# Optimization experiments

Hardware: AMD Instinct MI355X
Metric: run time of the kernel (lower is better)

The kernel has to match this reference:

```python
import jax, jax.numpy as jnp
import numpy as np

N_NODES = 100000
N_EDGES = 1600000
D = 256
N_QUERY = 50000

def setup_inputs() -> dict:
    key = jax.random.key(0)
    k1, k2, k3, k4, k5, k6 = jax.random.split(key, 6)
    embeddings = jax.random.normal(k1, (N_NODES, D), dtype=jnp.float32)
    edge_src = jax.random.randint(k2, (N_EDGES,), 0, N_NODES)
    edge_dst = jax.random.randint(k3, (N_EDGES,), 0, N_NODES)
    edge_w = jax.random.uniform(k4, (N_EDGES,), dtype=jnp.float32)
    node_ids = jax.random.randint(k5, (N_QUERY,), 0, N_NODES)
    # Xavier-uniform linear weight, zero bias (as in _init_weights)
    limit = float(np.sqrt(6.0 / (D + D)))
    W = jax.random.uniform(k6, (D, D), dtype=jnp.float32, minval=-limit, maxval=limit)
    b = jnp.zeros((D,), dtype=jnp.float32)
    return {"embeddings": embeddings, "edge_src": edge_src, "edge_dst": edge_dst,
            "edge_w": edge_w, "node_ids": node_ids, "W": W, "b": b}

def reference(embeddings, edge_src, edge_dst, edge_w, node_ids, W, b):
    # graph_convolution: sparse adj (COO) @ embeddings == scatter-add of weighted src rows into dst
    msgs = embeddings[edge_src] * edge_w[:, None]                # [E, D]
    agg = jax.ops.segment_sum(msgs, edge_dst, num_segments=N_NODES)  # [N, D]
    # predict_scores: gather queried nodes, apply linear classifier
    feats = agg[node_ids]                                        # [Q, D]
    return feats @ W.T + b                                       # [Q, D]
```

## Files before the change

### kernel.cpp

```cpp
#include <hip/hip_runtime.h>

#define D 256
#define TQ 32
#define GQ 64
#define NBW 3136

typedef __attribute__((ext_vector_type(8))) short short8;
typedef __attribute__((ext_vector_type(4))) short short4v;
typedef __attribute__((ext_vector_type(4))) float f32x4;

__device__ __forceinline__ unsigned short f2bf(float x) {
    unsigned int u = __float_as_uint(x);
    unsigned int r = (u + 0x7FFFu + ((u >> 16) & 1u)) >> 16;
    return (unsigned short)r;
}
__device__ __forceinline__ float bf2f(unsigned short h) {
    return __uint_as_float(((unsigned int)h) << 16);
}


__global__ __launch_bounds__(256) void convert_emb(
    const float4* __restrict__ emb, short8* __restrict__ embbf, int total8)
{
    int stride = gridDim.x * 256;
    for (int i = blockIdx.x * 256 + threadIdx.x; i < total8; i += stride) {
        float4 v0 = emb[(size_t)i * 2 + 0];
        float4 v1 = emb[(size_t)i * 2 + 1];
        short8 p;
        p[0] = (short)f2bf(v0.x); p[1] = (short)f2bf(v0.y);
        p[2] = (short)f2bf(v0.z); p[3] = (short)f2bf(v0.w);
        p[4] = (short)f2bf(v1.x); p[5] = (short)f2bf(v1.y);
        p[6] = (short)f2bf(v1.z); p[7] = (short)f2bf(v1.w);
        embbf[i] = p;
    }
}

__global__ __launch_bounds__(256) void convert_w(
    const float* __restrict__ W, unsigned short* __restrict__ Wbf)
{
    int i = blockIdx.x * 256 + threadIdx.x;
    const float4* src = (const float4*)W + (size_t)i * 2;
    float4 v0 = src[0];
    float4 v1 = src[1];
    short8 p;
    p[0] = (short)f2bf(v0.x); p[1] = (short)f2bf(v0.y);
    p[2] = (short)f2bf(v0.z); p[3] = (short)f2bf(v0.w);
    p[4] = (short)f2bf(v1.x); p[5] = (short)f2bf(v1.y);
    p[6] = (short)f2bf(v1.z); p[7] = (short)f2bf(v1.w);
    *((short8*)Wbf + i) = p;
}


__global__ __launch_bounds__(256) void flag_bits(
    const int* __restrict__ nid, unsigned int* __restrict__ bits, int Q)
{
    int q = blockIdx.x * 256 + threadIdx.x;
    if (q < Q) {
        int v = nid[q];
        atomicOr(&bits[v >> 5], 1u << (v & 31));
    }
}

__global__ __launch_bounds__(256) void hist_kernel(
    const int* __restrict__ edst, const unsigned int* __restrict__ bits,
    int* __restrict__ counts, int E)
{
    __shared__ unsigned int lb[NBW];
    for (int i = threadIdx.x; i < NBW; i += 256) lb[i] = bits[i];
    __syncthreads();
    int stride = gridDim.x * 256;
    for (int e = blockIdx.x * 256 + threadIdx.x; e < E; e += stride) {
        int d = edst[e];
        if ((lb[d >> 5] >> (d & 31)) & 1u) atomicAdd(&counts[d], 1);
    }
}

__global__ __launch_bounds__(256) void alloc_kernel(
    const int* __restrict__ counts, int* __restrict__ base,
    int* __restrict__ pos, int* __restrict__ total, int N)
{
    int n = blockIdx.x * 256 + threadIdx.x;
    if (n >= N) return;
    int c = counts[n];
    int b = 0;
    if (c > 0) b = atomicAdd(total, c);
    base[n] = b;
    pos[n]  = b;
}

__global__ __launch_bounds__(256) void bucket_kernel(
    const int* __restrict__ esrc, const int* __restrict__ edst,
    const float* __restrict__ ew, const unsigned int* __restrict__ bits,
    int* __restrict__ pos, int2* __restrict__ bucket, int E)
{
    __shared__ unsigned int lb[NBW];
    for (int i = threadIdx.x; i < NBW; i += 256) lb[i] = bits[i];
    __syncthreads();
    int stride = gridDim.x * 256;
    for (int e = blockIdx.x * 256 + threadIdx.x; e < E; e += stride) {
        int d = edst[e];
        if ((lb[d >> 5] >> (d & 31)) & 1u) {
            int idx = atomicAdd(&pos[d], 1);
            bucket[idx] = make_int2(esrc[e], __float_as_int(ew[e]));
        }
    }
}

__global__ __launch_bounds__(256) void accum_nodes(
    const short4v* __restrict__ embbf,
    const int2*    __restrict__ bucket,
    const int*     __restrict__ base,
    const int*     __restrict__ counts,
    const unsigned int* __restrict__ bits,
    short4v*       __restrict__ aggbf,
    int N)
{
    const int lane = threadIdx.x & 63;
    const int wid  = (int)((blockIdx.x * 256 + threadIdx.x) >> 6);
    if (wid >= N) return;
    if (!((bits[wid >> 5] >> (wid & 31)) & 1u)) return;

    const int b = base[wid];
    const int c = counts[wid];
    float a0 = 0.f, a1 = 0.f, a2 = 0.f, a3 = 0.f;

    int i = 0;
    for (; i + 8 <= c; i += 8) {
        #pragma unroll
        for (int u = 0; u < 8; ++u) {
            int2 s = bucket[b + i + u];
            short4v v = embbf[(size_t)s.x * 64 + lane];
            float w = __int_as_float(s.y);
            a0 += bf2f((unsigned short)v[0]) * w;
            a1 += bf2f((unsigned short)v[1]) * w;
            a2 += bf2f((unsigned short)v[2]) * w;
            a3 += bf2f((unsigned short)v[3]) * w;
        }
    }
    for (; i < c; ++i) {
        int2 s = bucket[b + i];
        short4v v = embbf[(size_t)s.x * 64 + lane];
        float w = __int_as_float(s.y);
        a0 += bf2f((unsigned short)v[0]) * w;
        a1 += bf2f((unsigned short)v[1]) * w;
        a2 += bf2f((unsigned short)v[2]) * w;
        a3 += bf2f((unsigned short)v[3]) * w;
    }
    short4v o;
    o[0] = (short)f2bf(a0); o[1] = (short)f2bf(a1);
    o[2] = (short)f2bf(a2); o[3] = (short)f2bf(a3);
    aggbf[(size_t)wid * 64 + lane] = o;
}

__global__ __launch_bounds__(256) void gather_gemm_mfma(
    const unsigned short* __restrict__ aggbf,
    const int* __restrict__ nid,
    const unsigned short* __restrict__ Wbf,
    const float* __restrict__ b,
    float* __restrict__ out, int Q)
{
    __shared__ unsigned char lds[GQ * 512];
    const int t  = threadIdx.x;
    const int q0 = blockIdx.x * GQ;

    #pragma unroll
    for (int s = 0; s < 8; ++s) {
        const int i   = t + s * 256;
        const int row = i >> 5;
        const int ch  = i & 31;
        const int q   = q0 + row;
        short8 p = {0, 0, 0, 0, 0, 0, 0, 0};
        if (q < Q) p = *((const short8*)aggbf + (size_t)nid[q] * 32 + ch);
        int byte = row * 512 + ch * 16;
        byte ^= (row & 7) << 4;
        *(short8*)(lds + byte) = p;
    }
    __syncthreads();

    const int wave = t >> 6;
    const int lane = t & 63;
    const int qw   = wave * 16;
    const int lrow = lane & 15;
    const int kg   = lane >> 4;

    short8 afrag[8];
    #pragma unroll
    for (int ks = 0; ks < 8; ++ks) {
        int byte = (qw + lrow) * 512 + ks * 64 + kg * 16;
        byte ^= ((qw + lrow) & 7) << 4;
        afrag[ks] = *(const short8*)(lds + byte);
    }

    const unsigned short* wp0 = Wbf + (size_t)lrow * 256 + kg * 8;

    for (int jt = 0; jt < 16; ++jt) {
        f32x4 acc = {0.f, 0.f, 0.f, 0.f};
        const unsigned short* wp = wp0 + (size_t)jt * 16 * 256;
        #pragma unroll
        for (int ks = 0; ks < 8; ++ks) {
            short8 bfrag = *(const short8*)(wp + ks * 32);
            acc = __builtin_amdgcn_mfma_f32_16x16x32_bf16(afrag[ks], bfrag, acc, 0, 0, 0);
        }
        const float bias = b[jt * 16 + lrow];
        #pragma unroll
        for (int r = 0; r < 4; ++r) {
            const int row = kg * 4 + r;
            const int q   = q0 + qw + row;
            if (q < Q) out[(size_t)q * D + jt * 16 + lrow] = acc[r] + bias;
        }
    }
}


__global__ __launch_bounds__(256) void scatter_edges(
    const float4* __restrict__ emb, const int* __restrict__ esrc,
    const int* __restrict__ edst, const float* __restrict__ ew,
    float* __restrict__ agg, int E)
{
    const int lane = threadIdx.x & 63;
    const int wid  = (int)((blockIdx.x * blockDim.x + threadIdx.x) >> 6);
    const int nw   = (int)((gridDim.x * blockDim.x) >> 6);
    for (int e = wid; e < E; e += nw) {
        const int   s = esrc[e];
        const int   d = edst[e];
        const float w = ew[e];
        float4 v = emb[(size_t)s * (D / 4) + lane];
        float* o = agg + (size_t)d * D + lane * 4;
        unsafeAtomicAdd(o + 0, v.x * w);
        unsafeAtomicAdd(o + 1, v.y * w);
        unsafeAtomicAdd(o + 2, v.z * w);
        unsafeAtomicAdd(o + 3, v.w * w);
    }
}

__global__ __launch_bounds__(256) void gather_gemm_w(
    const float* __restrict__ agg, const int* __restrict__ nid,
    const float* __restrict__ W, const float* __restrict__ b,
    float* __restrict__ out, int Q)
{
    __shared__ float fl[TQ][D];
    const int t  = threadIdx.x;
    const int q0 = blockIdx.x * TQ;

    for (int i = t; i < TQ * (D / 4); i += 256) {
        const int r = i >> 6;
        const int c = i & 63;
        const int q = q0 + r;
        float4 v = make_float4(0.f, 0.f, 0.f, 0.f);
        if (q < Q) v = ((const float4*)agg)[(size_t)nid[q] * (D / 4) + c];
        ((float4*)&fl[r][0])[c] = v;
    }
    __syncthreads();

    const int j = t;
    float acc[TQ];
    #pragma unroll
    for (int r = 0; r < TQ; ++r) acc[r] = 0.f;

    const float4* wr4 = (const float4*)(W + (size_t)j * D);
    for (int k4 = 0; k4 < D / 4; ++k4) {
        const float4 w4 = wr4[k4];
        #pragma unroll
        for (int r = 0; r < TQ; ++r) {
            const float4 f = ((const float4*)&fl[r][0])[k4];
            acc[r] += f.x * w4.x + f.y * w4.y + f.z * w4.z + f.w * w4.w;
        }
    }

    const float bias = b[j];
    #pragma unroll
    for (int r = 0; r < TQ; ++r) {
        const int q = q0 + r;
        if (q < Q) out[(size_t)q * D + j] = acc[r] + bias;
    }
}

extern "C" void kernel_launch(void* const* d_in, const int* in_sizes, int n_in,
                              void* d_out, int out_size, void* d_ws, size_t ws_size,
                              hipStream_t stream) {
    const float* emb  = (const float*)d_in[0];
    const int*   esrc = (const int*)d_in[1];
    const int*   edst = (const int*)d_in[2];
    const float* ew   = (const float*)d_in[3];
    const int*   nid  = (const int*)d_in[4];
    const float* W    = (const float*)d_in[5];
    const float* b    = (const float*)d_in[6];
    float*       out  = (float*)d_out;

    const int N = in_sizes[0] / D;
    const int E = in_sizes[1];
    const int Q = in_sizes[4];

    char* wsb = (char*)d_ws;

    size_t off_agg    = 0;
    size_t off_emb    = off_agg    + (size_t)N * D * 2;
    size_t off_counts = off_emb    + (size_t)N * D * 2;
    size_t off_base   = off_counts + (size_t)N * sizeof(int);
    size_t off_pos    = off_base   + (size_t)N * sizeof(int);
    size_t off_total  = off_pos    + (size_t)N * sizeof(int);
    size_t off_bits   = off_total  + 256;
    size_t off_bucket = off_bits   + (size_t)NBW * 4;
    size_t off_wbf    = off_bucket + (size_t)E * sizeof(int2);
    size_t needed     = off_wbf    + (size_t)D * D * 2;

    if (ws_size >= needed) {
        unsigned short* aggbf  = (unsigned short*)(wsb + off_agg);
        short8*         embbf  = (short8*)(wsb + off_emb);
        int*            counts = (int*)(wsb + off_counts);
        int*            basep  = (int*)(wsb + off_base);
        int*            pos    = (int*)(wsb + off_pos);
        int*            total  = (int*)(wsb + off_total);
        unsigned int*   bits   = (unsigned int*)(wsb + off_bits);
        int2*           bucket = (int2*)(wsb + off_bucket);
        unsigned short* Wbf    = (unsigned short*)(wsb + off_wbf);

        hipMemsetAsync(wsb + off_counts, 0, off_bucket - off_counts, stream);

        convert_emb  <<<2048, 256, 0, stream>>>((const float4*)emb, embbf, N * D / 8);
        convert_w    <<<32, 256, 0, stream>>>(W, Wbf);
        flag_bits    <<<(Q + 255) / 256, 256, 0, stream>>>(nid, bits, Q);
        hist_kernel  <<<2048, 256, 0, stream>>>(edst, bits, counts, E);
        alloc_kernel <<<(N + 255) / 256, 256, 0, stream>>>(counts, basep, pos, total, N);
        bucket_kernel<<<2048, 256, 0, stream>>>(esrc, edst, ew, bits, pos, bucket, E);

        int nb_acc = (int)(((size_t)N * 64 + 255) / 256);
        accum_nodes<<<nb_acc, 256, 0, stream>>>((const short4v*)embbf, bucket, basep,
                                                counts, bits, (short4v*)aggbf, N);

        const int nb = (Q + GQ - 1) / GQ;
        gather_gemm_mfma<<<nb, 256, 0, stream>>>(aggbf, nid, Wbf, b, out, Q);
    } else {
        float* agg = (float*)wsb;
        hipMemsetAsync(agg, 0, (size_t)N * D * sizeof(float), stream);
        scatter_edges<<<2048, 256, 0, stream>>>((const float4*)emb, esrc, edst, ew, agg, E);
        const int nb = (Q + TQ - 1) / TQ;
        gather_gemm_w<<<nb, 256, 0, stream>>>(agg, nid, W, b, out, Q);
    }
}
```

Baseline: 402.8 us.

## Split gather-GEMM per 16 queries across four waves by output column

The gather-GEMM kernel no longer stages 64 query rows in LDS. Each block now handles 16 queries, and each of its four waves loads the A fragments straight from global memory and computes a quarter of the 256 output columns. This removes the LDS staging and the barrier and launches four times as many blocks, which is meant to raise parallelism. The cost is that every gathered row is read four times from global memory or cache, once per wave.

After: 405.8 us. Within noise of the previous version (+0.8%).

```diff
diff --git a/kernel.cpp b/kernel.cpp
--- a/kernel.cpp
+++ b/kernel.cpp
@@ -2,7 +2,6 @@
 
 #define D 256
 #define TQ 32
-#define GQ 64
 #define NBW 3136
 
 typedef __attribute__((ext_vector_type(8))) short short8;
@@ -159,41 +158,27 @@
     const float* __restrict__ b,
     float* __restrict__ out, int Q)
 {
-    __shared__ unsigned char lds[GQ * 512];
-    const int t  = threadIdx.x;
-    const int q0 = blockIdx.x * GQ;
-
-    #pragma unroll
-    for (int s = 0; s < 8; ++s) {
-        const int i   = t + s * 256;
-        const int row = i >> 5;
-        const int ch  = i & 31;
-        const int q   = q0 + row;
-        short8 p = {0, 0, 0, 0, 0, 0, 0, 0};
-        if (q < Q) p = *((const short8*)aggbf + (size_t)nid[q] * 32 + ch);
-        int byte = row * 512 + ch * 16;
-        byte ^= (row & 7) << 4;
-        *(short8*)(lds + byte) = p;
-    }
-    __syncthreads();
-
-    const int wave = t >> 6;
-    const int lane = t & 63;
-    const int qw   = wave * 16;
+    const int lane = threadIdx.x & 63;
+    const int part = threadIdx.x >> 6;
+    const int rg   = blockIdx.x;
     const int lrow = lane & 15;
     const int kg   = lane >> 4;
 
+    const int qa = rg * 16 + lrow;
+    int node = 0;
+    if (qa < Q) node = nid[qa];
+    const unsigned short* ap = aggbf + (size_t)node * 256 + kg * 8;
+
     short8 afrag[8];
     #pragma unroll
-    for (int ks = 0; ks < 8; ++ks) {
-        int byte = (qw + lrow) * 512 + ks * 64 + kg * 16;
-        byte ^= ((qw + lrow) & 7) << 4;
-        afrag[ks] = *(const short8*)(lds + byte);
-    }
+    for (int ks = 0; ks < 8; ++ks)
+        afrag[ks] = *(const short8*)(ap + ks * 32);
 
     const unsigned short* wp0 = Wbf + (size_t)lrow * 256 + kg * 8;
 
-    for (int jt = 0; jt < 16; ++jt) {
+    #pragma unroll
+    for (int jj = 0; jj < 4; ++jj) {
+        const int jt = part * 4 + jj;
         f32x4 acc = {0.f, 0.f, 0.f, 0.f};
         const unsigned short* wp = wp0 + (size_t)jt * 16 * 256;
         #pragma unroll
@@ -205,8 +190,8 @@
         #pragma unroll
         for (int r = 0; r < 4; ++r) {
             const int row = kg * 4 + r;
-            const int q   = q0 + qw + row;
-            if (q < Q) out[(size_t)q * D + jt * 16 + lrow] = acc[r] + bias;
+            const int oq  = rg * 16 + row;
+            if (oq < Q) out[(size_t)oq * D + jt * 16 + lrow] = acc[r] + bias;
         }
     }
 }
@@ -328,7 +313,7 @@
         accum_nodes<<<nb_acc, 256, 0, stream>>>((const short4v*)embbf, bucket, basep,
                                                 counts, bits, (short4v*)aggbf, N);
 
-        const int nb = (Q + GQ - 1) / GQ;
+        const int nb = (Q + 15) / 16;
         gather_gemm_mfma<<<nb, 256, 0, stream>>>(aggbf, nid, Wbf, b, out, Q);
     } else {
         float* agg = (float*)wsb;
```
